# Optimization experiments

Measured on AMD Instinct MI355X. Metric: run time of the kernel, lower is better.

The kernel has to match this reference:

```python
import jax, jax.numpy as jnp
import numpy as np

N_NODES = 128   # num_nodes
BATCH = 4096
HIDDEN = 32     # fixed by the module's Linear(N+1, 32)


def setup_inputs() -> dict:
    key = jax.random.key(0)
    ks = jax.random.split(key, 8)
    N, B, H = N_NODES, BATCH, HIDDEN
    x = jax.random.normal(ks[0], (B, N), dtype=jnp.float32)
    # adjacency masks: A[b, :, j] = parent indicator of node j in sample b
    A = (jax.random.uniform(ks[1], (B, N, N)) < 0.3).astype(jnp.float32)
    # per-sample topological permutation
    order = jax.vmap(lambda k: jax.random.permutation(k, N))(
        jax.random.split(ks[2], B)).astype(jnp.int32)
    # intervention target per sample, -1 = no intervention
    do_idxs = jax.random.randint(ks[3], (B,), -1, N, dtype=jnp.int32)
    # externalized intervention noise (torch.normal in the original forward)
    u = jax.random.normal(ks[4], (B,), dtype=jnp.float32)
    # stacked per-node MLP params: Linear(N+1, 32) -> LeakyReLU -> Linear(32, 1)
    W1 = jax.random.normal(ks[5], (N, N + 1, H), dtype=jnp.float32) / np.sqrt(N + 1)
    b1 = jnp.zeros((N, H), dtype=jnp.float32)
    W2 = jax.random.normal(ks[6], (N, H, 1), dtype=jnp.float32) / np.sqrt(H)
    b2 = jnp.zeros((N, 1), dtype=jnp.float32)
    return dict(x=x, A=A, u=u, W1=W1, b1=b1, W2=W2, b2=b2,
                order=order, do_idxs=do_idxs)


def reference(x, A, u, W1, b1, W2, b2, order, do_idxs):
    B, N = x.shape
    bidx = jnp.arange(B)
    # set intervened entries: outputs[b, do_idxs[b]] = u[b] where do_idxs != -1
    outputs0 = jnp.where(do_idxs[:, None] == jnp.arange(N)[None, :],
                         u[:, None], jnp.zeros_like(x))

    def step(outputs, node):           # node: [B] current node per sample
        mask = A[bidx, :, node]        # [B, N] parent mask of this node
        ins = jnp.concatenate([mask * outputs,
                               x[bidx, node][:, None]], axis=1)  # [B, N+1]
        # per-node MLP gathered by node id (grouped tiny GEMMs)
        h = jax.nn.leaky_relu(jnp.einsum('bd,bdh->bh', ins, W1[node]) + b1[node])
        out = (jnp.einsum('bh,bho->bo', h, W2[node]) + b2[node])[:, 0]  # [B]
        # intervened samples keep their value u (they are skipped in the original)
        new_val = jnp.where(do_idxs == node, outputs[bidx, node], out)
        return outputs.at[bidx, node].set(new_val), None

    outputs, _ = jax.lax.scan(step, outputs0, order.T)  # sequential topo order
    return outputs
```

## Files before the change

### kernel.cpp

```cpp
#include <hip/hip_runtime.h>
#include <stdint.h>

#define NN 128
#define BB 4096
#define HH 32
#define SLOT_W 17
#define BATCH_W (NN * SLOT_W)

__global__ __launch_bounds__(256) void pack_bits(const float* __restrict__ A,
                                                 unsigned long long* __restrict__ bitsW) {
    int t = blockIdx.x * 256 + threadIdx.x;
    int n4 = t & 31;
    int h  = (t >> 5) & 1;
    int b  = t >> 6;
    const float4* Ap = (const float4*)(A + (size_t)b * NN * NN + (size_t)h * 64 * NN) + n4;
    unsigned long long m0 = 0, m1 = 0, m2 = 0, m3 = 0;
#pragma unroll 8
    for (int d = 0; d < 64; ++d) {
        float4 v = Ap[(size_t)d * (NN / 4)];
        unsigned long long bit = 1ull << d;
        if (v.x != 0.f) m0 |= bit;
        if (v.y != 0.f) m1 |= bit;
        if (v.z != 0.f) m2 |= bit;
        if (v.w != 0.f) m3 |= bit;
    }
    unsigned long long* dst = bitsW + ((size_t)b * NN + n4 * 4) * 2 + h;
    dst[0] = m0; dst[2] = m1; dst[4] = m2; dst[6] = m3;
}

__device__ __forceinline__ void fill_slot(uint8_t* s, int node,
                                          uint64_t m0, uint64_t m1) {
    int cnt = __popcll(m0) + __popcll(m1);
    s[1] = (uint8_t)node;
    if (cnt <= 56) {
        int c = 0;
        while (m0) { int d = __builtin_ctzll(m0); m0 &= m0 - 1; s[8 + c] = (uint8_t)d; ++c; }
        while (m1) { int d = __builtin_ctzll(m1); m1 &= m1 - 1; s[8 + c] = (uint8_t)(64 + d); ++c; }
        while (c & 7) { s[8 + c] = 128; ++c; }
        s[0] = (uint8_t)c;
    } else {
        s[0] = 255;
        uint32_t* mp = (uint32_t*)(s + 8);
        mp[0] = (uint32_t)m0; mp[1] = (uint32_t)(m0 >> 32);
        mp[2] = (uint32_t)m1; mp[3] = (uint32_t)(m1 >> 32);
    }
}

__global__ __launch_bounds__(256) void build_lists(
    const ulonglong2* __restrict__ bitsT, const int* __restrict__ order,
    const int* __restrict__ do_idxs, uint32_t* __restrict__ lists)
{
    __shared__ uint8_t slot[4][NN][68];
    const int wv = threadIdx.x >> 6, lane = threadIdx.x & 63;
    const int b = blockIdx.x * 4 + wv;
    const int na  = order[b * NN + lane];
    const int nb  = order[b * NN + 64 + lane];
    const int dob = do_idxs[b];

    uint64_t sa_lo = (na < 64) ? (1ull << na) : 0ull;
    uint64_t sa_hi = (na < 64) ? 0ull : (1ull << (na - 64));
    uint64_t sb_lo = (nb < 64) ? (1ull << nb) : 0ull;
    uint64_t sb_hi = (nb < 64) ? 0ull : (1ull << (nb - 64));
#pragma unroll
    for (int s = 1; s < 64; s <<= 1) {
        uint64_t t0 = __shfl_up(sa_lo, s), t1 = __shfl_up(sa_hi, s);
        uint64_t t2 = __shfl_up(sb_lo, s), t3 = __shfl_up(sb_hi, s);
        if (lane >= s) { sa_lo |= t0; sa_hi |= t1; sb_lo |= t2; sb_hi |= t3; }
    }
    uint64_t Pa_lo = __shfl_up(sa_lo, 1), Pa_hi = __shfl_up(sa_hi, 1);
    uint64_t Pb_lo = __shfl_up(sb_lo, 1), Pb_hi = __shfl_up(sb_hi, 1);
    if (lane == 0) { Pa_lo = 0; Pa_hi = 0; Pb_lo = 0; Pb_hi = 0; }
    const uint64_t f_lo = __shfl(sa_lo, 63), f_hi = __shfl(sa_hi, 63);
    Pb_lo |= f_lo; Pb_hi |= f_hi;
    if (dob >= 0) {
        uint64_t dlo = (dob < 64) ? (1ull << dob) : 0ull;
        uint64_t dhi = (dob < 64) ? 0ull : (1ull << (dob - 64));
        Pa_lo |= dlo; Pa_hi |= dhi; Pb_lo |= dlo; Pb_hi |= dhi;
    }
    const ulonglong2 ba = bitsT[(size_t)b * NN + na];
    const ulonglong2 bc = bitsT[(size_t)b * NN + nb];
    fill_slot(&slot[wv][lane][0],      na, Pa_lo & ba.x, Pa_hi & ba.y);
    fill_slot(&slot[wv][64 + lane][0], nb, Pb_lo & bc.x, Pb_hi & bc.y);
    __syncthreads();
    const uint32_t* src = (const uint32_t*)&slot[0][0][0];
    uint32_t* dst = lists + (size_t)blockIdx.x * (4 * BATCH_W);
    for (int i = threadIdx.x; i < 4 * BATCH_W; i += 256) dst[i] = src[i];
}

#define ENT8(k) { \
    uint32_t wb = (uint32_t)__builtin_amdgcn_ds_bpermute(baddr + ((k) << 3), (int)sv); \
    int d = (wb >> sh2) & 255; \
    float vv = vals[d]; \
    const float4 wr = *(const float4*)(Wp + (d << 5)); \
    acc.x = fmaf(vv, wr.x, acc.x); acc.y = fmaf(vv, wr.y, acc.y); \
    acc.z = fmaf(vv, wr.z, acc.z); acc.w = fmaf(vv, wr.w, acc.w); }

__global__ __launch_bounds__(64) void cond_mlp_list(
    const float* __restrict__ x, const float* __restrict__ u,
    const float* __restrict__ W1, const float* __restrict__ b1,
    const float* __restrict__ W2, const float* __restrict__ b2,
    const int* __restrict__ do_idxs, const uint32_t* __restrict__ lists,
    float* __restrict__ out)
{
    const int b = blockIdx.x;
    const int lane = threadIdx.x;
    const int jj = (lane & 7) << 2;
    const int sh2 = lane & 24;
    const int baddr = (2 + (lane >> 5)) << 2;
    const int q = lane >> 3;

    __shared__ float vals[132];
    const int dob = do_idxs[b];
    const float ub = u[b];
    vals[lane]      = (lane == dob) ? ub : 0.f;
    vals[64 + lane] = (lane + 64 == dob) ? ub : 0.f;
    if (lane < 4) vals[128 + lane] = 0.f;

    const uint32_t* sp = lists + (size_t)b * BATCH_W;
    uint32_t sv = sp[lane & 15];

    for (int t = 0; t < NN; ++t) {
        const int tn = (t < NN - 1) ? t + 1 : t;
        const uint32_t sv_n = sp[tn * SLOT_W + (lane & 15)];

        const uint32_t w0 = (uint32_t)__builtin_amdgcn_readfirstlane((int)sv);
        const int cnt  = w0 & 255;
        const int node = (w0 >> 8) & 255;

        const float* __restrict__ Wp = W1 + (size_t)node * ((NN + 1) * HH) + jj;
        const float4 wx  = *(const float4*)(Wp + NN * HH);
        const float4 b1q = *(const float4*)(b1 + (node << 5) + jj);
        const float4 w2q = *(const float4*)(W2 + (node << 5) + jj);
        const float  xv  = x[(b << 7) + node];
        const float  b2v = b2[node];

        float4 acc = make_float4(0.f, 0.f, 0.f, 0.f);
        if (cnt != 255) {
            switch (cnt >> 3) {
            case 7: ENT8(6); case 6: ENT8(5); case 5: ENT8(4);
            case 4: ENT8(3); case 3: ENT8(2); case 2: ENT8(1);
            case 1: ENT8(0); case 0: ;
            }
        } else {
            uint32_t mw0 = (uint32_t)__builtin_amdgcn_readlane((int)sv, 2);
            uint32_t mw1 = (uint32_t)__builtin_amdgcn_readlane((int)sv, 3);
            uint32_t mw2 = (uint32_t)__builtin_amdgcn_readlane((int)sv, 4);
            uint32_t mw3 = (uint32_t)__builtin_amdgcn_readlane((int)sv, 5);
            uint64_t m0 = mw0 | ((uint64_t)mw1 << 32);
            uint64_t m1 = mw2 | ((uint64_t)mw3 << 32);
            int i = 0;
            while (m0) {
                int d = __builtin_ctzll(m0); m0 &= m0 - 1;
                float vv = ((i & 7) == q) ? vals[d] : 0.f;
                const float4 wr = *(const float4*)(Wp + (d << 5));
                acc.x = fmaf(vv, wr.x, acc.x); acc.y = fmaf(vv, wr.y, acc.y);
                acc.z = fmaf(vv, wr.z, acc.z); acc.w = fmaf(vv, wr.w, acc.w);
                ++i;
            }
            while (m1) {
                int d = 64 + __builtin_ctzll(m1); m1 &= m1 - 1;
                float vv = ((i & 7) == q) ? vals[d] : 0.f;
                const float4 wr = *(const float4*)(Wp + (d << 5));
                acc.x = fmaf(vv, wr.x, acc.x); acc.y = fmaf(vv, wr.y, acc.y);
                acc.z = fmaf(vv, wr.z, acc.z); acc.w = fmaf(vv, wr.w, acc.w);
                ++i;
            }
        }

        acc.x += __shfl_xor(acc.x, 32); acc.y += __shfl_xor(acc.y, 32);
        acc.z += __shfl_xor(acc.z, 32); acc.w += __shfl_xor(acc.w, 32);
        acc.x += __shfl_xor(acc.x, 16); acc.y += __shfl_xor(acc.y, 16);
        acc.z += __shfl_xor(acc.z, 16); acc.w += __shfl_xor(acc.w, 16);
        acc.x += __shfl_xor(acc.x, 8);  acc.y += __shfl_xor(acc.y, 8);
        acc.z += __shfl_xor(acc.z, 8);  acc.w += __shfl_xor(acc.w, 8);

        acc.x = fmaf(xv, wx.x, acc.x) + b1q.x;
        acc.y = fmaf(xv, wx.y, acc.y) + b1q.y;
        acc.z = fmaf(xv, wx.z, acc.z) + b1q.z;
        acc.w = fmaf(xv, wx.w, acc.w) + b1q.w;

        float4 h;
        h.x = fmaxf(acc.x, 0.01f * acc.x);
        h.y = fmaxf(acc.y, 0.01f * acc.y);
        h.z = fmaxf(acc.z, 0.01f * acc.z);
        h.w = fmaxf(acc.w, 0.01f * acc.w);

        float p = h.x * w2q.x + h.y * w2q.y + h.z * w2q.z + h.w * w2q.w;
        p += __shfl_xor(p, 4);
        p += __shfl_xor(p, 2);
        p += __shfl_xor(p, 1);
        const float outv = p + b2v;

        if (node != dob) {
            if (lane == 0) vals[node] = outv;
        }
        sv = sv_n;
    }

    out[(b << 7) + lane]      = vals[lane];
    out[(b << 7) + 64 + lane] = vals[64 + lane];
}

__global__ __launch_bounds__(64) void cond_mlp_ballot(
    const float* __restrict__ x, const float* __restrict__ u,
    const float* __restrict__ W1, const float* __restrict__ b1,
    const float* __restrict__ W2, const float* __restrict__ b2,
    const int* __restrict__ order, const int* __restrict__ do_idxs,
    const ulonglong2* __restrict__ bitsT, float* __restrict__ out)
{
    const int b = blockIdx.x;
    const int lane = threadIdx.x;
    const int j = lane & 31;
    const int half = lane >> 5;

    __shared__ float2 ent[132];

    const float ub = u[b];
    const int dob = do_idxs[b];
    float out0 = (dob == lane) ? ub : 0.f;
    float out1 = (dob == lane + 64) ? ub : 0.f;

    const int* ord = order + b * NN;
    const ulonglong2* bb = bitsT + (size_t)b * NN;

    int node = ord[0];
    ulonglong2 bits = bb[node];

    for (int t = 0; t < NN; ++t) {
        const int node_n = (t < NN - 1) ? ord[t + 1] : 0;
        const ulonglong2 bits_n = bb[node_n];

        const float* Wn = W1 + (size_t)node * (NN + 1) * HH;
        const float w2v = W2[node * HH + j];
        const float b1v = b1[node * HH + j];
        const float xv  = x[b * NN + node];
        const float b2v = b2[node];

        unsigned long long bal0 = __ballot(out0 != 0.f) & bits.x;
        unsigned long long bal1 = __ballot(out1 != 0.f) & bits.y;
        const int c0 = __popcll(bal0);
        const int cnt = c0 + __popcll(bal1);
        const unsigned long long below = (1ull << lane) - 1;
        if (bal0 & (1ull << lane)) {
            int p = __popcll(bal0 & below);
            ent[p] = make_float2(out0, __int_as_float(lane));
        }
        if (bal1 & (1ull << lane)) {
            int p = c0 + __popcll(bal1 & below);
            ent[p] = make_float2(out1, __int_as_float(lane + 64));
        }
        const int cnt4 = (cnt + 3) & ~3;
        if (lane < cnt4 - cnt) ent[cnt + lane] = make_float2(0.f, __int_as_float(0));
        __syncthreads();

        float acc0 = 0.f, acc1 = 0.f;
        for (int k = 0; k < cnt4; k += 4) {
            float2 eA = ent[k + half];
            float2 eB = ent[k + 2 + half];
            acc0 += eA.x * Wn[__float_as_int(eA.y) * HH + j];
            acc1 += eB.x * Wn[__float_as_int(eB.y) * HH + j];
        }
        __syncthreads();

        float acc = acc0 + acc1;
        acc += __shfl_xor(acc, 32);
        acc += xv * Wn[NN * HH + j];
        acc += b1v;
        const float hv = (acc > 0.f) ? acc : 0.01f * acc;

        float p = hv * w2v;
        p += __shfl_xor(p, 16);
        p += __shfl_xor(p, 8);
        p += __shfl_xor(p, 4);
        p += __shfl_xor(p, 2);
        p += __shfl_xor(p, 1);
        const float outv = p + b2v;

        if (dob != node) {
            if (lane == (node & 63)) {
                if (node < 64) out0 = outv; else out1 = outv;
            }
        }
        node = node_n;
        bits = bits_n;
    }

    out[b * NN + lane] = out0;
    out[b * NN + 64 + lane] = out1;
}

extern "C" void kernel_launch(void* const* d_in, const int* in_sizes, int n_in,
                              void* d_out, int out_size, void* d_ws, size_t ws_size,
                              hipStream_t stream) {
    const float* x   = (const float*)d_in[0];
    const float* A   = (const float*)d_in[1];
    const float* u   = (const float*)d_in[2];
    const float* W1  = (const float*)d_in[3];
    const float* b1  = (const float*)d_in[4];
    const float* W2  = (const float*)d_in[5];
    const float* b2  = (const float*)d_in[6];
    const int* order = (const int*)d_in[7];
    const int* dox   = (const int*)d_in[8];

    unsigned long long* bitsW = (unsigned long long*)d_ws;
    uint32_t* lists = (uint32_t*)((uint8_t*)d_ws + (size_t)8 * 1024 * 1024);
    const size_t need = (size_t)8 * 1024 * 1024 + (size_t)BB * NN * 68;

    pack_bits<<<(BB * 64) / 256, 256, 0, stream>>>(A, bitsW);
    if (ws_size >= need) {
        build_lists<<<BB / 4, 256, 0, stream>>>((const ulonglong2*)bitsW, order, dox, lists);
        cond_mlp_list<<<BB, 64, 0, stream>>>(x, u, W1, b1, W2, b2, dox, lists, (float*)d_out);
    } else {
        cond_mlp_ballot<<<BB, 64, 0, stream>>>(x, u, W1, b1, W2, b2, order, dox,
                                               (const ulonglong2*)bitsW, (float*)d_out);
    }
}
```

Before: 565.2 us.

## Software-pipeline W1 row gathers one step ahead and use DPP reductions

Restructures the per-sample sequential loop into a two-stage software pipeline. The parent-index decode and W1 row gathers for the next node are issued before the current node's MLP is consumed, which hides global-load latency behind the dependent chain. The small xor-1/2/4/8 reductions now use DPP intrinsics instead of ds_bpermute shuffles, and launch bounds request 4 waves per EU. In exchange, the doubled float4 prefetch arrays raise register pressure, which can hurt occupancy or cause spills.

```diff
diff --git a/kernel.cpp b/kernel.cpp
--- a/kernel.cpp
+++ b/kernel.cpp
@@ -87,15 +87,103 @@
     for (int i = threadIdx.x; i < 4 * BATCH_W; i += 256) dst[i] = src[i];
 }
 
-#define ENT8(k) { \
-    uint32_t wb = (uint32_t)__builtin_amdgcn_ds_bpermute(baddr + ((k) << 3), (int)sv); \
-    int d = (wb >> sh2) & 255; \
-    float vv = vals[d]; \
-    const float4 wr = *(const float4*)(Wp + (d << 5)); \
-    acc.x = fmaf(vv, wr.x, acc.x); acc.y = fmaf(vv, wr.y, acc.y); \
-    acc.z = fmaf(vv, wr.z, acc.z); acc.w = fmaf(vv, wr.w, acc.w); }
-
-__global__ __launch_bounds__(64) void cond_mlp_list(
+__device__ __forceinline__ float dppadd_xor1(float v) {
+    int t = __builtin_amdgcn_update_dpp(0, __float_as_int(v), 0xB1, 0xF, 0xF, true);
+    return v + __int_as_float(t);
+}
+__device__ __forceinline__ float dppadd_xor2(float v) {
+    int t = __builtin_amdgcn_update_dpp(0, __float_as_int(v), 0x4E, 0xF, 0xF, true);
+    return v + __int_as_float(t);
+}
+__device__ __forceinline__ float dppadd_xor4(float v) {
+    int t = __builtin_amdgcn_update_dpp(0, __float_as_int(v), 0x141, 0xF, 0xF, true);
+    return v + __int_as_float(t);
+}
+__device__ __forceinline__ float dppadd_xor8(float v) {
+    int t = __builtin_amdgcn_update_dpp(0, __float_as_int(v), 0x128, 0xF, 0xF, true);
+    return v + __int_as_float(t);
+}
+
+#define PREF(cnt_, node_, wb_, w_, m0_, m1_, svv) do {                        \
+    uint32_t w0_ = (uint32_t)__builtin_amdgcn_readfirstlane((int)(svv));      \
+    cnt_ = w0_ & 255; node_ = (w0_ >> 8) & 255;                               \
+    if (cnt_ != 255) {                                                        \
+        const float* Wp_ = W1 + (size_t)node_ * 4128 + jj;                    \
+        _Pragma("unroll")                                                     \
+        for (int k_ = 0; k_ < 7; ++k_) {                                      \
+            if (k_ * 8 < cnt_) {                                              \
+                wb_[k_] = (uint32_t)__builtin_amdgcn_ds_bpermute(             \
+                    baddr + (k_ << 3), (int)(svv));                           \
+                int d_ = (wb_[k_] >> sh2) & 255;                              \
+                w_[k_] = *(const float4*)(Wp_ + (d_ << 5));                   \
+            }                                                                 \
+        }                                                                     \
+    } else {                                                                  \
+        uint32_t a_ = (uint32_t)__builtin_amdgcn_readlane((int)(svv), 2);     \
+        uint32_t b_ = (uint32_t)__builtin_amdgcn_readlane((int)(svv), 3);     \
+        uint32_t c_ = (uint32_t)__builtin_amdgcn_readlane((int)(svv), 4);     \
+        uint32_t e_ = (uint32_t)__builtin_amdgcn_readlane((int)(svv), 5);     \
+        m0_ = a_ | ((uint64_t)b_ << 32);                                      \
+        m1_ = c_ | ((uint64_t)e_ << 32);                                      \
+    }                                                                         \
+} while (0)
+
+#define CONS(cnt_, node_, wb_, w_, m0_, m1_) do {                             \
+    const float* Wp_ = W1 + (size_t)node_ * 4128 + jj;                        \
+    const float4 wx_  = *(const float4*)(Wp_ + 4096);                         \
+    const float4 b1q_ = *(const float4*)(b1 + (node_ << 5) + jj);             \
+    const float4 w2q_ = *(const float4*)(W2 + (node_ << 5) + jj);             \
+    const float  xv_  = x[(b << 7) + node_];                                  \
+    const float  b2v_ = b2[node_];                                            \
+    float4 acc = make_float4(0.f, 0.f, 0.f, 0.f);                             \
+    if (cnt_ != 255) {                                                        \
+        _Pragma("unroll")                                                     \
+        for (int k_ = 0; k_ < 7; ++k_) {                                      \
+            if (k_ * 8 < cnt_) {                                              \
+                int d_ = (wb_[k_] >> sh2) & 255;                              \
+                float vv_ = vals[d_];                                         \
+                acc.x = fmaf(vv_, w_[k_].x, acc.x);                           \
+                acc.y = fmaf(vv_, w_[k_].y, acc.y);                           \
+                acc.z = fmaf(vv_, w_[k_].z, acc.z);                           \
+                acc.w = fmaf(vv_, w_[k_].w, acc.w);                           \
+            }                                                                 \
+        }                                                                     \
+    } else {                                                                  \
+        uint64_t mm0 = m0_, mm1 = m1_; int i_ = 0;                            \
+        while (mm0) { int d_ = __builtin_ctzll(mm0); mm0 &= mm0 - 1;          \
+            float vv_ = ((i_ & 7) == q) ? vals[d_] : 0.f;                     \
+            const float4 wr_ = *(const float4*)(Wp_ + (d_ << 5));             \
+            acc.x = fmaf(vv_, wr_.x, acc.x); acc.y = fmaf(vv_, wr_.y, acc.y); \
+            acc.z = fmaf(vv_, wr_.z, acc.z); acc.w = fmaf(vv_, wr_.w, acc.w); \
+            ++i_; }                                                           \
+        while (mm1) { int d_ = 64 + __builtin_ctzll(mm1); mm1 &= mm1 - 1;     \
+            float vv_ = ((i_ & 7) == q) ? vals[d_] : 0.f;                     \
+            const float4 wr_ = *(const float4*)(Wp_ + (d_ << 5));             \
+            acc.x = fmaf(vv_, wr_.x, acc.x); acc.y = fmaf(vv_, wr_.y, acc.y); \
+            acc.z = fmaf(vv_, wr_.z, acc.z); acc.w = fmaf(vv_, wr_.w, acc.w); \
+            ++i_; }                                                           \
+    }                                                                         \
+    acc.x += __shfl_xor(acc.x, 32); acc.y += __shfl_xor(acc.y, 32);           \
+    acc.z += __shfl_xor(acc.z, 32); acc.w += __shfl_xor(acc.w, 32);           \
+    acc.x += __shfl_xor(acc.x, 16); acc.y += __shfl_xor(acc.y, 16);           \
+    acc.z += __shfl_xor(acc.z, 16); acc.w += __shfl_xor(acc.w, 16);           \
+    acc.x = dppadd_xor8(acc.x); acc.y = dppadd_xor8(acc.y);                   \
+    acc.z = dppadd_xor8(acc.z); acc.w = dppadd_xor8(acc.w);                   \
+    acc.x = fmaf(xv_, wx_.x, acc.x) + b1q_.x;                                 \
+    acc.y = fmaf(xv_, wx_.y, acc.y) + b1q_.y;                                 \
+    acc.z = fmaf(xv_, wx_.z, acc.z) + b1q_.z;                                 \
+    acc.w = fmaf(xv_, wx_.w, acc.w) + b1q_.w;                                 \
+    float hx_ = fmaxf(acc.x, 0.01f * acc.x), hy_ = fmaxf(acc.y, 0.01f * acc.y); \
+    float hz_ = fmaxf(acc.z, 0.01f * acc.z), hw_ = fmaxf(acc.w, 0.01f * acc.w); \
+    float p_ = hx_ * w2q_.x + hy_ * w2q_.y + hz_ * w2q_.z + hw_ * w2q_.w;     \
+    p_ = dppadd_xor1(p_);                                                     \
+    p_ = dppadd_xor2(p_);                                                     \
+    p_ = dppadd_xor4(p_);                                                     \
+    const float outv_ = p_ + b2v_;                                            \
+    if (node_ != dob) { if (lane == 0) vals[node_] = outv_; }                 \
+} while (0)
+
+__global__ __launch_bounds__(64, 4) void cond_mlp_list(
     const float* __restrict__ x, const float* __restrict__ u,
     const float* __restrict__ W1, const float* __restrict__ b1,
     const float* __restrict__ W2, const float* __restrict__ b2,
@@ -108,6 +196,7 @@
     const int sh2 = lane & 24;
     const int baddr = (2 + (lane >> 5)) << 2;
     const int q = lane >> 3;
+    const int wslot = lane & 15;
 
     __shared__ float vals[132];
     const int dob = do_idxs[b];
@@ -117,84 +206,27 @@
     if (lane < 4) vals[128 + lane] = 0.f;
 
     const uint32_t* sp = lists + (size_t)b * BATCH_W;
-    uint32_t sv = sp[lane & 15];
-
-    for (int t = 0; t < NN; ++t) {
-        const int tn = (t < NN - 1) ? t + 1 : t;
-        const uint32_t sv_n = sp[tn * SLOT_W + (lane & 15)];
-
-        const uint32_t w0 = (uint32_t)__builtin_amdgcn_readfirstlane((int)sv);
-        const int cnt  = w0 & 255;
-        const int node = (w0 >> 8) & 255;
-
-        const float* __restrict__ Wp = W1 + (size_t)node * ((NN + 1) * HH) + jj;
-        const float4 wx  = *(const float4*)(Wp + NN * HH);
-        const float4 b1q = *(const float4*)(b1 + (node << 5) + jj);
-        const float4 w2q = *(const float4*)(W2 + (node << 5) + jj);
-        const float  xv  = x[(b << 7) + node];
-        const float  b2v = b2[node];
-
-        float4 acc = make_float4(0.f, 0.f, 0.f, 0.f);
-        if (cnt != 255) {
-            switch (cnt >> 3) {
-            case 7: ENT8(6); case 6: ENT8(5); case 5: ENT8(4);
-            case 4: ENT8(3); case 3: ENT8(2); case 2: ENT8(1);
-            case 1: ENT8(0); case 0: ;
-            }
-        } else {
-            uint32_t mw0 = (uint32_t)__builtin_amdgcn_readlane((int)sv, 2);
-            uint32_t mw1 = (uint32_t)__builtin_amdgcn_readlane((int)sv, 3);
-            uint32_t mw2 = (uint32_t)__builtin_amdgcn_readlane((int)sv, 4);
-            uint32_t mw3 = (uint32_t)__builtin_amdgcn_readlane((int)sv, 5);
-            uint64_t m0 = mw0 | ((uint64_t)mw1 << 32);
-            uint64_t m1 = mw2 | ((uint64_t)mw3 << 32);
-            int i = 0;
-            while (m0) {
-                int d = __builtin_ctzll(m0); m0 &= m0 - 1;
-                float vv = ((i & 7) == q) ? vals[d] : 0.f;
-                const float4 wr = *(const float4*)(Wp + (d << 5));
-                acc.x = fmaf(vv, wr.x, acc.x); acc.y = fmaf(vv, wr.y, acc.y);
-                acc.z = fmaf(vv, wr.z, acc.z); acc.w = fmaf(vv, wr.w, acc.w);
-                ++i;
-            }
-            while (m1) {
-                int d = 64 + __builtin_ctzll(m1); m1 &= m1 - 1;
-                float vv = ((i & 7) == q) ? vals[d] : 0.f;
-                const float4 wr = *(const float4*)(Wp + (d << 5));
-                acc.x = fmaf(vv, wr.x, acc.x); acc.y = fmaf(vv, wr.y, acc.y);
-                acc.z = fmaf(vv, wr.z, acc.z); acc.w = fmaf(vv, wr.w, acc.w);
-                ++i;
-            }
-        }
-
-        acc.x += __shfl_xor(acc.x, 32); acc.y += __shfl_xor(acc.y, 32);
-        acc.z += __shfl_xor(acc.z, 32); acc.w += __shfl_xor(acc.w, 32);
-        acc.x += __shfl_xor(acc.x, 16); acc.y += __shfl_xor(acc.y, 16);
-        acc.z += __shfl_xor(acc.z, 16); acc.w += __shfl_xor(acc.w, 16);
-        acc.x += __shfl_xor(acc.x, 8);  acc.y += __shfl_xor(acc.y, 8);
-        acc.z += __shfl_xor(acc.z, 8);  acc.w += __shfl_xor(acc.w, 8);
-
-        acc.x = fmaf(xv, wx.x, acc.x) + b1q.x;
-        acc.y = fmaf(xv, wx.y, acc.y) + b1q.y;
-        acc.z = fmaf(xv, wx.z, acc.z) + b1q.z;
-        acc.w = fmaf(xv, wx.w, acc.w) + b1q.w;
-
-        float4 h;
-        h.x = fmaxf(acc.x, 0.01f * acc.x);
-        h.y = fmaxf(acc.y, 0.01f * acc.y);
-        h.z = fmaxf(acc.z, 0.01f * acc.z);
-        h.w = fmaxf(acc.w, 0.01f * acc.w);
-
-        float p = h.x * w2q.x + h.y * w2q.y + h.z * w2q.z + h.w * w2q.w;
-        p += __shfl_xor(p, 4);
-        p += __shfl_xor(p, 2);
-        p += __shfl_xor(p, 1);
-        const float outv = p + b2v;
-
-        if (node != dob) {
-            if (lane == 0) vals[node] = outv;
-        }
-        sv = sv_n;
+
+    int Acnt, Anode, Bcnt, Bnode;
+    uint32_t Awb[7], Bwb[7];
+    float4 Aw[7], Bw[7];
+    uint64_t Am0 = 0, Am1 = 0, Bm0 = 0, Bm1 = 0;
+
+    uint32_t A_sv = sp[wslot];
+    uint32_t B_sv = sp[SLOT_W + wslot];
+    PREF(Acnt, Anode, Awb, Aw, Am0, Am1, A_sv);
+
+    for (int t = 0; t < NN; t += 2) {
+        const int t2 = (t + 2 < NN) ? t + 2 : NN - 1;
+        const int t3 = (t + 3 < NN) ? t + 3 : NN - 1;
+        const uint32_t C_sv = sp[t2 * SLOT_W + wslot];
+        const uint32_t D_sv = sp[t3 * SLOT_W + wslot];
+
+        PREF(Bcnt, Bnode, Bwb, Bw, Bm0, Bm1, B_sv);
+        CONS(Acnt, Anode, Awb, Aw, Am0, Am1);
+        PREF(Acnt, Anode, Awb, Aw, Am0, Am1, C_sv);
+        CONS(Bcnt, Bnode, Bwb, Bw, Bm0, Bm1);
+        B_sv = D_sv;
     }
 
     out[(b << 7) + lane]      = vals[lane];
```

Result: faster. 547.3 us (-3.2%).
